# Performance work log

Measured on AMD Instinct MI355X. Metric: run time of the kernel, lower is better.

## Reference

```python
import jax, jax.numpy as jnp
import numpy as np

# Log-signature at depth m=3, d channels, expressed in the full tensor basis
# (iisignature 'expanded' convention; the Lyndon-basis output of method '' is a
# fixed linear projection of these coefficients).

def _chen_step(carry, dx):
    # carry: signature levels S1 [B,d], S2 [B,d,d], S3 [B,d,d,d]
    # dx: increment of one segment, [B,d]. Segment signature E = exp(dx).
    S1, S2, S3 = carry
    E2 = 0.5 * jnp.einsum('bi,bj->bij', dx, dx)
    E3 = (1.0 / 6.0) * jnp.einsum('bi,bj,bk->bijk', dx, dx, dx)
    nS1 = S1 + dx
    nS2 = S2 + jnp.einsum('bi,bj->bij', S1, dx) + E2
    nS3 = (S3
           + jnp.einsum('bij,bk->bijk', S2, dx)
           + jnp.einsum('bi,bjk->bijk', S1, E2)
           + E3)
    return (nS1, nS2, nS3), None


def _logsig(x):
    # x: [B, L, d] path. Returns expanded log-signature [B, d + d^2 + d^3].
    B, L, d = x.shape
    dx = jnp.swapaxes(x[:, 1:] - x[:, :-1], 0, 1)  # [L-1, B, d]
    init = (jnp.zeros((B, d), x.dtype),
            jnp.zeros((B, d, d), x.dtype),
            jnp.zeros((B, d, d, d), x.dtype))
    (S1, S2, S3), _ = jax.lax.scan(_chen_step, init, dx)
    # log(1 + S) truncated at level 3 in the tensor algebra
    l1 = S1
    l2 = S2 - 0.5 * jnp.einsum('bi,bj->bij', S1, S1)
    l3 = (S3
          - 0.5 * (jnp.einsum('bi,bjk->bijk', S1, S2)
                   + jnp.einsum('bij,bk->bijk', S2, S1))
          + (1.0 / 3.0) * jnp.einsum('bi,bj,bk->bijk', S1, S1, S1))
    return jnp.concatenate(
        [l1.reshape(B, -1), l2.reshape(B, -1), l3.reshape(B, -1)], axis=-1)


def setup_inputs() -> dict:
    key = jax.random.key(0)
    B, L, d = 2048, 256, 8
    steps = 0.1 * jax.random.normal(key, (B, L, d), dtype=jnp.float32)
    x = jnp.cumsum(steps, axis=1)  # random-walk paths keep signatures well-scaled
    return {"x": x}


def reference(x):
    return _logsig(x)
```

## Files before the change

kernel.cpp:

```cpp
#include <hip/hip_runtime.h>


#define LEN 256
#define DCH 8
#define NW 4
#define CHUNK (LEN / NW)
#define OUTSTRIDE (DCH + DCH*DCH + DCH*DCH*DCH)

typedef _Float16 h8 __attribute__((ext_vector_type(8)));
typedef _Float16 h4 __attribute__((ext_vector_type(4)));

__global__ __launch_bounds__(256) void logsig_fused(const float* __restrict__ x,
                                                    float* __restrict__ out) {
    __shared__ __align__(16) unsigned char pool[LEN * DCH * 4];
    __shared__ __align__(16) _Float16 dxh[LEN][DCH];
    __shared__ __align__(16) float sig1[NW][8];
    __shared__ __align__(16) float sig2[NW][64];
    __shared__ __align__(16) float s1buf[8];
    __shared__ __align__(16) float s2buf[64];

    float (*dxbuf)[DCH] = (float(*)[DCH])pool;
    float (*sig3)[512]  = (float(*)[512])pool;

    const int tid  = threadIdx.x;
    const int w    = tid >> 6;
    const int lane = tid & 63;
    const int i    = lane >> 3;
    const int j    = lane & 7;
    const int b    = blockIdx.x;

    const float4* x4 = (const float4*)(x + (size_t)b * (LEN * DCH));
    float4* d4 = (float4*)&dxbuf[0][0];
    h4* dh4 = (h4*)&dxh[0][0];
    for (int f = tid; f < 512; f += 256) {
        float4 dv;
        if (f < 510) {
            float4 a = x4[f];
            float4 c = x4[f + 2];
            dv.x = c.x - a.x; dv.y = c.y - a.y; dv.z = c.z - a.z; dv.w = c.w - a.w;
        } else {
            dv.x = 0.f; dv.y = 0.f; dv.z = 0.f; dv.w = 0.f;
        }
        d4[f] = dv;
        h4 hv = { (_Float16)dv.x, (_Float16)dv.y, (_Float16)dv.z, (_Float16)dv.w };
        dh4[f] = hv;
    }
    __syncthreads();

    float s1 = 0.f, s2 = 0.f;
    float s3[8];
#pragma unroll
    for (int k = 0; k < 8; ++k) s3[k] = 0.f;

    const float c6 = 1.f / 6.f;
    const float* base = &dxbuf[w * CHUNK][0];
    const h8* hbase = (const h8*)&dxh[w * CHUNK][0];

    for (int tb = 0; tb < CHUNK; tb += 4) {
#pragma unroll
        for (int u = 0; u < 4; ++u) {
            const int t = tb + u;
            const float* row = base + t * 8;
            h8 hr = hbase[t];
            float dxi = row[i];
            float dxj = row[j];
            float tt = fmaf(c6, dxi, 0.5f * s1);
            float w3 = fmaf(tt, dxj, s2);
#pragma unroll
            for (int k = 0; k < 8; ++k)
                s3[k] = fmaf(w3, (float)hr[k], s3[k]);
            float uu = fmaf(0.5f, dxi, s1);
            s2 = fmaf(uu, dxj, s2);
            s1 += dxi;
        }
    }

    __syncthreads();

    if (j == 0) sig1[w][i] = s1;
    sig2[w][lane] = s2;
    float* sp = &sig3[w][lane * 8];
    *(float4*)(sp)     = make_float4(s3[0], s3[1], s3[2], s3[3]);
    *(float4*)(sp + 4) = make_float4(s3[4], s3[5], s3[6], s3[7]);
    __syncthreads();

    if (w != 0) return;

    for (int c = 1; c < NW; ++c) {
        float B1i  = sig1[c][i];
        float B1j  = sig1[c][j];
        float B2ij = sig2[c][lane];
        float4 b1a = *(const float4*)&sig1[c][0];
        float4 b1b = *(const float4*)&sig1[c][4];
        const float* b2row = &sig2[c][j * 8];
        float4 b2a = *(const float4*)(b2row);
        float4 b2b = *(const float4*)(b2row + 4);
        const float* b3row = &sig3[c][lane * 8];
        float4 b3a = *(const float4*)(b3row);
        float4 b3b = *(const float4*)(b3row + 4);
        float B1k[8]  = {b1a.x, b1a.y, b1a.z, b1a.w, b1b.x, b1b.y, b1b.z, b1b.w};
        float B2jk[8] = {b2a.x, b2a.y, b2a.z, b2a.w, b2b.x, b2b.y, b2b.z, b2b.w};
        float B3[8]   = {b3a.x, b3a.y, b3a.z, b3a.w, b3b.x, b3b.y, b3b.z, b3b.w};
#pragma unroll
        for (int k = 0; k < 8; ++k)
            s3[k] = s3[k] + B3[k] + s1 * B2jk[k] + s2 * B1k[k];
        s2 = s2 + B2ij + s1 * B1j;
        s1 = s1 + B1i;
    }

    if (j == 0) s1buf[i] = s1;
    s2buf[lane] = s2;

    float S1r[8], S2rj[8];
#pragma unroll
    for (int k = 0; k < 8; ++k) S1r[k] = s1buf[k];
#pragma unroll
    for (int k = 0; k < 8; ++k) S2rj[k] = s2buf[j * 8 + k];
    float s1j = s1buf[j];

    float* ob = out + (size_t)b * OUTSTRIDE;
    if (lane < 8) ob[lane] = s1buf[lane];
    ob[8 + lane] = fmaf(-0.5f * s1, s1j, s2);

    float c3 = (1.f / 3.f) * s1 * s1j;
    float l3[8];
#pragma unroll
    for (int k = 0; k < 8; ++k)
        l3[k] = s3[k] - 0.5f * (s1 * S2rj[k] + s2 * S1r[k]) + c3 * S1r[k];
    float* p3 = ob + 72 + lane * 8;
    *(float4*)(p3)     = make_float4(l3[0], l3[1], l3[2], l3[3]);
    *(float4*)(p3 + 4) = make_float4(l3[4], l3[5], l3[6], l3[7]);
}

extern "C" void kernel_launch(void* const* d_in, const int* in_sizes, int n_in,
                              void* d_out, int out_size, void* d_ws, size_t ws_size,
                              hipStream_t stream) {
    const float* x = (const float*)d_in[0];
    float* out = (float*)d_out;
    const int B = in_sizes[0] / (LEN * DCH);
    hipLaunchKernelGGL(logsig_fused, dim3(B), dim3(256), 0, stream, x, out);
}
```

Baseline: 78.47 us.

## Transpose fp32 increments in LDS and use fma_mix for level-3 accumulation

```diff
diff --git a/kernel.cpp b/kernel.cpp
--- a/kernel.cpp
+++ b/kernel.cpp
@@ -6,21 +6,29 @@
 #define NW 4
 #define CHUNK (LEN / NW)
 #define OUTSTRIDE (DCH + DCH*DCH + DCH*DCH*DCH)
+#define TSTRIDE 260
 
-typedef _Float16 h8 __attribute__((ext_vector_type(8)));
+typedef float f4v __attribute__((ext_vector_type(4)));
 typedef _Float16 h4 __attribute__((ext_vector_type(4)));
+
+#define MIX_LO(acc, wv, dw) \
+    asm("v_fma_mix_f32 %0, %1, %2, %0 op_sel:[0,0,0] op_sel_hi:[0,1,0]" \
+        : "+v"(acc) : "v"(wv), "v"(dw))
+#define MIX_HI(acc, wv, dw) \
+    asm("v_fma_mix_f32 %0, %1, %2, %0 op_sel:[0,1,0] op_sel_hi:[0,1,0]" \
+        : "+v"(acc) : "v"(wv), "v"(dw))
 
 __global__ __launch_bounds__(256) void logsig_fused(const float* __restrict__ x,
                                                     float* __restrict__ out) {
-    __shared__ __align__(16) unsigned char pool[LEN * DCH * 4];
+    __shared__ __align__(16) unsigned char pool[DCH * TSTRIDE * 4];
     __shared__ __align__(16) _Float16 dxh[LEN][DCH];
     __shared__ __align__(16) float sig1[NW][8];
     __shared__ __align__(16) float sig2[NW][64];
     __shared__ __align__(16) float s1buf[8];
     __shared__ __align__(16) float s2buf[64];
 
-    float (*dxbuf)[DCH] = (float(*)[DCH])pool;
-    float (*sig3)[512]  = (float(*)[512])pool;
+    float* dxT = (float*)pool;
+    float (*sig3)[512] = (float(*)[512])pool;
 
     const int tid  = threadIdx.x;
     const int w    = tid >> 6;
@@ -30,8 +38,6 @@
     const int b    = blockIdx.x;
 
     const float4* x4 = (const float4*)(x + (size_t)b * (LEN * DCH));
-    float4* d4 = (float4*)&dxbuf[0][0];
-    h4* dh4 = (h4*)&dxh[0][0];
     for (int f = tid; f < 512; f += 256) {
         float4 dv;
         if (f < 510) {
@@ -41,9 +47,14 @@
         } else {
             dv.x = 0.f; dv.y = 0.f; dv.z = 0.f; dv.w = 0.f;
         }
-        d4[f] = dv;
+        const int t  = f >> 1;
+        const int cg = (f & 1) * 4;
         h4 hv = { (_Float16)dv.x, (_Float16)dv.y, (_Float16)dv.z, (_Float16)dv.w };
-        dh4[f] = hv;
+        *(h4*)&dxh[t][cg] = hv;
+        dxT[(cg + 0) * TSTRIDE + t] = dv.x;
+        dxT[(cg + 1) * TSTRIDE + t] = dv.y;
+        dxT[(cg + 2) * TSTRIDE + t] = dv.z;
+        dxT[(cg + 3) * TSTRIDE + t] = dv.w;
     }
     __syncthreads();
 
@@ -53,23 +64,27 @@
     for (int k = 0; k < 8; ++k) s3[k] = 0.f;
 
     const float c6 = 1.f / 6.f;
-    const float* base = &dxbuf[w * CHUNK][0];
-    const h8* hbase = (const h8*)&dxh[w * CHUNK][0];
+    const int cb = w * CHUNK;
+    const uint32_t* hrow = (const uint32_t*)&dxh[cb][0];
+    const float* ti = dxT + i * TSTRIDE + cb;
+    const float* tj = dxT + j * TSTRIDE + cb;
 
-    for (int tb = 0; tb < CHUNK; tb += 4) {
+    for (int g = 0; g < 16; ++g) {
+        f4v qi = *(const f4v*)(ti + g * 4);
+        f4v qj = *(const f4v*)(tj + g * 4);
 #pragma unroll
         for (int u = 0; u < 4; ++u) {
-            const int t = tb + u;
-            const float* row = base + t * 8;
-            h8 hr = hbase[t];
-            float dxi = row[i];
-            float dxj = row[j];
-            float tt = fmaf(c6, dxi, 0.5f * s1);
+            const int t = g * 4 + u;
+            uint4 rw = *(const uint4*)(hrow + t * 4);
+            const float dxi = qi[u];
+            const float dxj = qj[u];
+            const float tt = fmaf(c6, dxi, 0.5f * s1);
             float w3 = fmaf(tt, dxj, s2);
-#pragma unroll
-            for (int k = 0; k < 8; ++k)
-                s3[k] = fmaf(w3, (float)hr[k], s3[k]);
-            float uu = fmaf(0.5f, dxi, s1);
+            MIX_LO(s3[0], w3, rw.x);  MIX_HI(s3[1], w3, rw.x);
+            MIX_LO(s3[2], w3, rw.y);  MIX_HI(s3[3], w3, rw.y);
+            MIX_LO(s3[4], w3, rw.z);  MIX_HI(s3[5], w3, rw.z);
+            MIX_LO(s3[6], w3, rw.w);  MIX_HI(s3[7], w3, rw.w);
+            const float uu = fmaf(0.5f, dxi, s1);
             s2 = fmaf(uu, dxj, s2);
             s1 += dxi;
         }
```

After: 75.00 us. -4.4%, faster.
